# Performance work log

Measured on AMD Instinct MI355X. Metric: run time of the kernel, lower is better.

## Reference

```python
import jax, jax.numpy as jnp
import numpy as np
from jax import lax

B, C, H, W = 4, 64, 256, 256
CH = C // 2  # attention hidden channels


def conv2d_same(x, w, b):
    # x: [B,Ci,H,W], w: [Co,Ci,kh,kw]
    y = lax.conv_general_dilated(x, w, (1, 1), 'SAME',
                                 dimension_numbers=('NCHW', 'OIHW', 'NCHW'))
    return y + b[None, :, None, None]


def conv1x1(x, w):
    # w: [Co,Ci]
    return jnp.einsum('oi,bihw->bohw', w, x)


def irnn_scan(x, w, b, axis, reverse):
    """Directional IRNN: h_t = relu(x_t + w_c * h_{t-1} + b_c), per channel.
    axis: 2 (rows/H) or 3 (cols/W). reverse=True scans from the far edge
    (e.g. bottom-to-top for 'up', right-to-left for 'left')."""
    xs = jnp.moveaxis(x, axis, 0)            # [L, B, C, rest]
    wb = w[None, :, None]                    # broadcast over [B, C, rest]
    bb = b[None, :, None]

    def step(h, xt):
        h = jax.nn.relu(xt + wb * h + bb)
        return h, h

    h0 = jnp.zeros_like(xs[0])
    _, ys = lax.scan(step, h0, xs, reverse=reverse)
    return jnp.moveaxis(ys, 0, axis)


def setup_inputs() -> dict:
    key = jax.random.key(0)
    ks = jax.random.split(key, 16)
    d = {}
    d['x'] = jax.random.normal(ks[0], (B, C, H, W), dtype=jnp.float32)
    # conv_in: 1x1, no bias
    d['w_in'] = jax.random.normal(ks[1], (C, C), dtype=jnp.float32) * 0.05
    # IRNN depthwise 1x1 weights (init alpha=1.0 in torch) + biases
    for i, name in enumerate(['up', 'right', 'down', 'left']):
        d['w_' + name] = jnp.ones((C,), dtype=jnp.float32)
        d['b_' + name] = jax.random.normal(ks[2 + i], (C,), dtype=jnp.float32) * 0.01
    # convD2: 1x1, 4C -> C, no bias
    d['wD2'] = jax.random.normal(ks[6], (C, 4 * C), dtype=jnp.float32) * 0.01
    # attention layers
    d['a1_w'] = jax.random.normal(ks[7], (CH, C, 3, 3), dtype=jnp.float32) * 0.05
    d['a1_b'] = jnp.zeros((CH,), dtype=jnp.float32)
    d['a2_w'] = jax.random.normal(ks[8], (CH, CH, 3, 3), dtype=jnp.float32) * 0.05
    d['a2_b'] = jnp.zeros((CH,), dtype=jnp.float32)
    d['a3_w'] = jax.random.normal(ks[9], (1, CH), dtype=jnp.float32) * 0.05
    d['a3_b'] = jnp.zeros((1,), dtype=jnp.float32)
    return d


def reference(x, w_in, w_up, b_up, w_right, b_right, w_down, b_down,
              w_left, b_left, wD2, a1_w, a1_b, a2_w, a2_b, a3_w, a3_b):
    out = conv1x1(x, w_in)
    # four directional spatial IRNN scans
    top_up = irnn_scan(out, w_up, b_up, axis=2, reverse=True)     # bottom->top
    top_right = irnn_scan(out, w_right, b_right, axis=3, reverse=False)  # left->right
    top_down = irnn_scan(out, w_down, b_down, axis=2, reverse=False)     # top->bottom
    top_left = irnn_scan(out, w_left, b_left, axis=3, reverse=True)      # right->left
    cat = jnp.concatenate([top_up, top_right, top_down, top_left], axis=1)  # [B,4C,H,W]
    out = jax.nn.relu(conv1x1(cat, wD2))
    # attention gate
    a = jax.nn.relu(conv2d_same(out, a1_w, a1_b))
    a = jax.nn.relu(conv2d_same(a, a2_w, a2_b))
    a = conv1x1(a, a3_w) + a3_b[None, :, None, None]
    weight = jax.nn.sigmoid(a)                # [B,1,H,W]
    return jax.nn.relu(x * weight)
```

## Files before the change

### kernel.cpp

```cpp
#include <hip/hip_runtime.h>
#include <hip/hip_bf16.h>

#define HWSZ  65536

typedef unsigned short ushort_t;
typedef unsigned int   uint_t;
typedef __attribute__((ext_vector_type(8))) _Float16 half8;
typedef __attribute__((ext_vector_type(2))) _Float16 half2v;
typedef __attribute__((ext_vector_type(4))) float f32x4;

static __device__ __forceinline__ void gl_lds16(const void* g, void* l) {
    __builtin_amdgcn_global_load_lds(
        (const __attribute__((address_space(1))) unsigned int*)g,
        (__attribute__((address_space(3))) unsigned int*)l, 16, 0, 0);
}

__global__ __launch_bounds__(256) void k1_mfma(
    const float* __restrict__ x, const float* __restrict__ w_in,
    _Float16* __restrict__ out0)
{
    __shared__ float xs[64][64];
    __shared__ _Float16 ah[64][72];
    __shared__ _Float16 al[64][72];
    int b   = blockIdx.x >> 10;
    int hw0 = (blockIdx.x & 1023) << 6;
    const float* xb = x + ((size_t)b * 64) * HWSZ + hw0;
    int wave = threadIdx.x >> 6, lane = threadIdx.x & 63;
    int n16 = lane & 15, quad = lane >> 4;

    for (int idx = threadIdx.x; idx < 1024; idx += 256) {
        int i = idx >> 4, p4 = (idx & 15) << 2;
        *(float4*)&xs[i][p4] = *(const float4*)(xb + (size_t)i * HWSZ + p4);
    }

    half8 Bh[2], Bl[2];
#pragma unroll
    for (int s = 0; s < 2; s++) {
        const float* wp = w_in + (wave * 16 + n16) * 64 + s * 32 + quad * 8;
#pragma unroll
        for (int j = 0; j < 8; j++) {
            float v = wp[j];
            _Float16 h = (_Float16)v;
            float r = v - (float)h;
            Bh[s][j] = h; Bl[s][j] = (_Float16)r;
        }
    }
    __syncthreads();

    {
        int px  = threadIdx.x & 63;
        int ic0 = (threadIdx.x >> 6) << 4;
        half8 h0, h1, l0, l1;
#pragma unroll
        for (int e = 0; e < 8; e++) {
            float v = xs[ic0 + e][px];
            _Float16 h = (_Float16)v;
            h0[e] = h; l0[e] = (_Float16)(v - (float)h);
        }
#pragma unroll
        for (int e = 0; e < 8; e++) {
            float v = xs[ic0 + 8 + e][px];
            _Float16 h = (_Float16)v;
            h1[e] = h; l1[e] = (_Float16)(v - (float)h);
        }
        *(half8*)&ah[px][ic0]     = h0;
        *(half8*)&ah[px][ic0 + 8] = h1;
        *(half8*)&al[px][ic0]     = l0;
        *(half8*)&al[px][ic0 + 8] = l1;
    }
    __syncthreads();

    f32x4 acc[4] = {};
#pragma unroll
    for (int j = 0; j < 4; j++) {
        int px = j * 16 + n16;
#pragma unroll
        for (int s = 0; s < 2; s++) {
            half8 Ah = *(const half8*)&ah[px][s * 32 + quad * 8];
            half8 Al = *(const half8*)&al[px][s * 32 + quad * 8];
            acc[j] = __builtin_amdgcn_mfma_f32_16x16x32_f16(Ah, Bh[s], acc[j], 0, 0, 0);
            acc[j] = __builtin_amdgcn_mfma_f32_16x16x32_f16(Al, Bh[s], acc[j], 0, 0, 0);
            acc[j] = __builtin_amdgcn_mfma_f32_16x16x32_f16(Ah, Bl[s], acc[j], 0, 0, 0);
        }
    }
    _Float16* ob = out0 + ((size_t)b * HWSZ + hw0) * 64 + wave * 16;
#pragma unroll
    for (int j = 0; j < 4; j++)
#pragma unroll
        for (int r = 0; r < 4; r++) {
            int px = j * 16 + quad * 4 + r;
            ob[(size_t)px * 64 + n16] = (_Float16)acc[j][r];
        }
}

__global__ __launch_bounds__(256) void k2_scan(
    const _Float16* __restrict__ out0,
    const float* __restrict__ w_up, const float* __restrict__ b_up,
    const float* __restrict__ w_rt, const float* __restrict__ b_rt,
    const float* __restrict__ w_dn, const float* __restrict__ b_dn,
    const float* __restrict__ w_lf, const float* __restrict__ b_lf,
    _Float16* __restrict__ cat)
{
    int c2 = threadIdx.x & 31;
    int q  = threadIdx.x >> 5;
    int dir = blockIdx.x >> 7;
    int bid = blockIdx.x & 127;
    int b = bid >> 5, g = bid & 31;
    int line = g * 8 + q;
    size_t base = (size_t)b * HWSZ;
    bool vert = dir < 2;
    bool rev  = dir & 1;

    const float *wp, *bp; int coff;
    if      (dir == 0) { wp = w_dn; bp = b_dn; coff = 128; }
    else if (dir == 1) { wp = w_up; bp = b_up; coff = 0;   }
    else if (dir == 2) { wp = w_rt; bp = b_rt; coff = 64;  }
    else               { wp = w_lf; bp = b_lf; coff = 192; }
    float w0v = wp[2 * c2], b0v = bp[2 * c2];
    float w1v = wp[2 * c2 + 1], b1v = bp[2 * c2 + 1];
    int coff2 = coff >> 1;

    const half2v* src = (const half2v*)out0;
    half2v* dst = (half2v*)cat;

    float h0 = 0.f, h1 = 0.f;
    for (int k0 = 0; k0 < 256; k0 += 16) {
        half2v v[16];
#pragma unroll
        for (int jx = 0; jx < 16; jx++) {
            int i = rev ? 255 - (k0 + jx) : (k0 + jx);
            size_t pix = vert ? (base + i * 256 + line) : (base + line * 256 + i);
            v[jx] = src[pix * 32 + c2];
        }
#pragma unroll
        for (int jx = 0; jx < 16; jx++) {
            int i = rev ? 255 - (k0 + jx) : (k0 + jx);
            size_t pix = vert ? (base + i * 256 + line) : (base + line * 256 + i);
            h0 = fmaxf(0.f, (float)v[jx][0] + w0v * h0 + b0v);
            h1 = fmaxf(0.f, (float)v[jx][1] + w1v * h1 + b1v);
            half2v o; o[0] = (_Float16)h0; o[1] = (_Float16)h1;
            dst[pix * 128 + coff2 + c2] = o;
        }
    }
}

__global__ __launch_bounds__(256) void packall(
    const float* __restrict__ wD2, const float* __restrict__ a1w,
    const float* __restrict__ a2w,
    _Float16* __restrict__ wf, _Float16* __restrict__ p1,
    _Float16* __restrict__ p2)
{
    int i = blockIdx.x * 256 + threadIdx.x;
    if (i < 16384) {
        wf[i] = (_Float16)wD2[i];
        return;
    }
    int k = i - 16384;
    if (k < 18432) {
        int j = k & 7, lane = (k >> 3) & 63, st = k >> 9;
        int s = st >> 1, t = st & 1;
        int oc = t * 16 + (lane & 15);
        int gk = s * 32 + (lane >> 4) * 8 + j;
        int dydx = gk >> 6, ic = gk & 63;
        p1[k] = (_Float16)a1w[((oc * 64 + ic) * 3 + dydx / 3) * 3 + dydx % 3];
    } else if (k < 27648) {
        int e = k - 18432;
        int j = e & 7, lane = (e >> 3) & 63, st = e >> 9;
        int s = st >> 1, t = st & 1;
        int oc = t * 16 + (lane & 15);
        int gk = s * 32 + (lane >> 4) * 8 + j;
        int dydx = gk >> 5, ic = gk & 31;
        p2[e] = (_Float16)a2w[((oc * 32 + ic) * 3 + dydx / 3) * 3 + dydx % 3];
    }
}

__global__ __launch_bounds__(256) void k3_mfma(
    const _Float16* __restrict__ cat, const _Float16* __restrict__ wf,
    _Float16* __restrict__ out3)
{
    __shared__ _Float16 As[64 * 256];
    int wave = threadIdx.x >> 6, lane = threadIdx.x & 63;
    int n16 = lane & 15, quad = lane >> 4;
    size_t p0 = (size_t)blockIdx.x * 64;

    half8 B[8];
#pragma unroll
    for (int s = 0; s < 8; s++)
        B[s] = *(const half8*)(wf + (size_t)(wave * 16 + n16) * 256 + s * 32 + quad * 8);

#pragma unroll
    for (int it = 0; it < 8; it++) {
        int px = wave * 16 + it * 2 + (lane >> 5);
        int pu = lane & 31;
        int lu = pu ^ (px & 7);
        const _Float16* gp = cat + ((p0 + px) << 8) + lu * 8;
        _Float16* lp = As + wave * 4096 + it * 512;
        gl_lds16(gp, lp);
    }
    __syncthreads();

    f32x4 acc[4] = {};
#pragma unroll
    for (int j = 0; j < 4; j++) {
        int px = j * 16 + n16;
        const _Float16* lrow = As + px * 256;
        int x7 = px & 7;
#pragma unroll
        for (int s = 0; s < 8; s++) {
            int phys = (s * 4 + quad) ^ x7;
            half8 a = *(const half8*)(lrow + phys * 8);
            acc[j] = __builtin_amdgcn_mfma_f32_16x16x32_f16(a, B[s], acc[j], 0, 0, 0);
        }
    }

#pragma unroll
    for (int j = 0; j < 4; j++)
#pragma unroll
        for (int r = 0; r < 4; r++) {
            size_t op = (p0 + j * 16 + quad * 4 + r) * 64 + wave * 16 + n16;
            out3[op] = (_Float16)fmaxf(acc[j][r], 0.f);
        }
}

template <int IC>
__global__ __launch_bounds__(256) void convmfma(
    const _Float16* __restrict__ in, const _Float16* __restrict__ pb,
    const float* __restrict__ bias, _Float16* __restrict__ oh)
{
    constexpr int UPX = IC / 8;
    constexpr int KST = IC / 32;
    constexpr int PPS = 64 / UPX;
    __shared__ _Float16 Ls[6 * 66 * IC];

    int wave = threadIdx.x >> 6, lane = threadIdx.x & 63;
    int n16 = lane & 15, quad = lane >> 4;
    int bid = blockIdx.x;
    int bb  = bid >> 8;
    int hh0 = ((bid >> 2) & 63) << 2;
    int w0  = (bid & 3) << 6;
    const _Float16* ib = in + (size_t)bb * HWSZ * IC;

#pragma unroll
    for (int it = 0; it < (6 * UPX) / 4; it++) {
        int q   = it * 4 + wave;
        int r   = q / UPX, seg = q % UPX;
        int gh  = hh0 - 1 + r;
        int pxr = seg * PPS + lane / UPX;
        int pu  = lane % UPX;
        int px_lin = r * 66 + 1 + pxr;
        int lu  = (UPX == 8) ? (pu ^ (px_lin & 7)) : pu;
        _Float16* lp = Ls + (size_t)(r * 66 + 1 + seg * PPS) * IC;
        if ((unsigned)gh < 256u) {
            const _Float16* gp = ib + ((size_t)(gh * 256 + w0 + pxr)) * IC + lu * 8;
            gl_lds16(gp, lp);
        } else {
            half8 z = {};
            *(half8*)(lp + (size_t)lane * 8) = z;
        }
    }
    if (threadIdx.x < 12 * UPX) {
        int pu = threadIdx.x % UPX;
        int ph = threadIdx.x / UPX;
        int r = ph >> 1, side = ph & 1;
        int col = side ? 65 : 0;
        int gh = hh0 - 1 + r;
        int gw = w0 - 1 + side * 65;
        int px_lin = r * 66 + col;
        int lu = (UPX == 8) ? (pu ^ (px_lin & 7)) : pu;
        half8 v = {};
        if ((unsigned)gh < 256u && (unsigned)gw < 256u)
            v = *(const half8*)(ib + ((size_t)(gh * 256 + gw)) * IC + lu * 8);
        *(half8*)(Ls + (size_t)px_lin * IC + pu * 8) = v;
    }
    __syncthreads();

    f32x4 acc[4][2] = {};
#pragma unroll
    for (int dydx = 0; dydx < 9; dydx++) {
        int dy = dydx / 3, dx = dydx % 3;
        int r_lds = wave + dy;
#pragma unroll
        for (int kst = 0; kst < KST; kst++) {
            int s = dydx * KST + kst;
            half8 B0 = *(const half8*)(pb + (size_t)((s * 2 + 0) * 64 + lane) * 8);
            half8 B1 = *(const half8*)(pb + (size_t)((s * 2 + 1) * 64 + lane) * 8);
            int u = kst * 4 + quad;
#pragma unroll
            for (int j = 0; j < 4; j++) {
                int px_lin = r_lds * 66 + j * 16 + n16 + dx;
                int phys = (UPX == 8) ? (u ^ (px_lin & 7)) : u;
                half8 A = *(const half8*)(Ls + (size_t)px_lin * IC + phys * 8);
                acc[j][0] = __builtin_amdgcn_mfma_f32_16x16x32_f16(A, B0, acc[j][0], 0, 0, 0);
                acc[j][1] = __builtin_amdgcn_mfma_f32_16x16x32_f16(A, B1, acc[j][1], 0, 0, 0);
            }
        }
    }

    int hh = hh0 + wave;
#pragma unroll
    for (int t = 0; t < 2; t++) {
        float bv = bias[t * 16 + n16];
#pragma unroll
        for (int j = 0; j < 4; j++)
#pragma unroll
            for (int r = 0; r < 4; r++) {
                int wp = w0 + j * 16 + quad * 4 + r;
                size_t op = ((size_t)bb * HWSZ + hh * 256 + wp) * 32 + t * 16 + n16;
                oh[op] = (_Float16)fmaxf(acc[j][t][r] + bv, 0.f);
            }
    }
}

__global__ __launch_bounds__(256) void k6_gate(
    const _Float16* __restrict__ a2, const float* __restrict__ a3w,
    const float* __restrict__ a3b, const float* __restrict__ x,
    float* __restrict__ out)
{
    int pix = blockIdx.x * 256 + threadIdx.x;
    int b = pix >> 16;
    int hw = pix & 65535;
    const _Float16* ap = a2 + (size_t)pix * 32;
    half8 q0 = *(const half8*)(ap);
    half8 q1 = *(const half8*)(ap + 8);
    half8 q2 = *(const half8*)(ap + 16);
    half8 q3 = *(const half8*)(ap + 24);
    float s = a3b[0];
#pragma unroll
    for (int j = 0; j < 8; j++) {
        s += a3w[j]      * (float)q0[j];
        s += a3w[j + 8]  * (float)q1[j];
        s += a3w[j + 16] * (float)q2[j];
        s += a3w[j + 24] * (float)q3[j];
    }
    float g = 1.f / (1.f + __expf(-s));
    const float* xb = x + (size_t)b * 64 * HWSZ + hw;
    float* ob = out + (size_t)b * 64 * HWSZ + hw;
#pragma unroll 8
    for (int c = 0; c < 64; c++)
        ob[(size_t)c * HWSZ] = fmaxf(0.f, xb[(size_t)c * HWSZ] * g);
}

extern "C" void kernel_launch(void* const* d_in, const int* in_sizes, int n_in,
                              void* d_out, int out_size, void* d_ws, size_t ws_size,
                              hipStream_t stream)
{
    const float* x     = (const float*)d_in[0];
    const float* w_in  = (const float*)d_in[1];
    const float* w_up  = (const float*)d_in[2];
    const float* b_up  = (const float*)d_in[3];
    const float* w_rt  = (const float*)d_in[4];
    const float* b_rt  = (const float*)d_in[5];
    const float* w_dn  = (const float*)d_in[6];
    const float* b_dn  = (const float*)d_in[7];
    const float* w_lf  = (const float*)d_in[8];
    const float* b_lf  = (const float*)d_in[9];
    const float* wD2   = (const float*)d_in[10];
    const float* a1w   = (const float*)d_in[11];
    const float* a1b   = (const float*)d_in[12];
    const float* a2w   = (const float*)d_in[13];
    const float* a2b   = (const float*)d_in[14];
    const float* a3w   = (const float*)d_in[15];
    const float* a3b   = (const float*)d_in[16];
    float* out = (float*)d_out;

    char* ws = (char*)d_ws;
    _Float16* out0 = (_Float16*)ws;
    _Float16* out3 = (_Float16*)ws;
    _Float16* wf16 = (_Float16*)(ws + (33ull << 20));
    _Float16* p1   = (_Float16*)(ws + (34ull << 20));
    _Float16* p2   = (_Float16*)(ws + (35ull << 20));
    _Float16* cat  = (_Float16*)(ws + (64ull << 20));
    _Float16* a1   = (_Float16*)(ws + (64ull << 20));
    _Float16* a2   = (_Float16*)(ws + (80ull << 20));

    k1_mfma   <<<4096, 256, 0, stream>>>(x, w_in, out0);
    k2_scan   <<<512,  256, 0, stream>>>(out0, w_up, b_up, w_rt, b_rt,
                                         w_dn, b_dn, w_lf, b_lf, cat);
    packall   <<<172,  256, 0, stream>>>(wD2, a1w, a2w, wf16, p1, p2);
    k3_mfma   <<<4096, 256, 0, stream>>>(cat, wf16, out3);
    convmfma<64><<<1024, 256, 0, stream>>>(out3, p1, a1b, a1);
    convmfma<32><<<1024, 256, 0, stream>>>(a1, p2, a2b, a2);
    k6_gate   <<<1024, 256, 0, stream>>>(a2, a3w, a3b, x, out);
}
```

Before: 268.3 us.

## Parallelize IRNN scan along sequence with chunked max-affine composition

Each scan line is split into 8 chunks of 32 steps, one per wavefront. Each chunk first computes a composable summary of the relu-affine recurrence, h -> max(M, S*h + T), and stores it in LDS. After a barrier, each chunk folds the summaries of the chunks before it to get its starting state, then rescans its 32 steps and writes the outputs. This raises the grid from 512 to 4096 blocks to break the long serial dependency chain, at the cost of reading the input twice. The composition is exact for relu(w*h + x + b), but the float ordering differs slightly from a plain sequential scan.

```diff
diff --git a/kernel.cpp b/kernel.cpp
--- a/kernel.cpp
+++ b/kernel.cpp
@@ -101,12 +101,12 @@
     const float* __restrict__ w_lf, const float* __restrict__ b_lf,
     _Float16* __restrict__ cat)
 {
+    __shared__ float comb[8][32][6];
     int c2 = threadIdx.x & 31;
-    int q  = threadIdx.x >> 5;
-    int dir = blockIdx.x >> 7;
-    int bid = blockIdx.x & 127;
-    int b = bid >> 5, g = bid & 31;
-    int line = g * 8 + q;
+    int ck = threadIdx.x >> 5;
+    int dir  = blockIdx.x >> 10;
+    int b    = (blockIdx.x >> 8) & 3;
+    int line = blockIdx.x & 255;
     size_t base = (size_t)b * HWSZ;
     bool vert = dir < 2;
     bool rev  = dir & 1;
@@ -123,25 +123,44 @@
     const half2v* src = (const half2v*)out0;
     half2v* dst = (half2v*)cat;
 
+#define PIXOF(k) (vert ? (base + (size_t)(rev ? 255 - (k) : (k)) * 256 + line) \
+                       : (base + line * 256 + (size_t)(rev ? 255 - (k) : (k))))
+
+    int k0 = ck << 5;
+
+    float M0 = -3e38f, S0 = 1.f, T0 = 0.f;
+    float M1 = -3e38f, S1 = 1.f, T1 = 0.f;
+#pragma unroll
+    for (int j = 0; j < 32; j++) {
+        half2v v = src[PIXOF(k0 + j) * 32 + c2];
+        float c0 = (float)v[0] + b0v;
+        float c1 = (float)v[1] + b1v;
+        M0 = fmaxf(0.f, fmaf(w0v, M0, c0));
+        T0 = fmaf(w0v, T0, c0);
+        S0 *= w0v;
+        M1 = fmaxf(0.f, fmaf(w1v, M1, c1));
+        T1 = fmaf(w1v, T1, c1);
+        S1 *= w1v;
+    }
+    comb[ck][c2][0] = M0; comb[ck][c2][1] = S0; comb[ck][c2][2] = T0;
+    comb[ck][c2][3] = M1; comb[ck][c2][4] = S1; comb[ck][c2][5] = T1;
+    __syncthreads();
+
     float h0 = 0.f, h1 = 0.f;
-    for (int k0 = 0; k0 < 256; k0 += 16) {
-        half2v v[16];
-#pragma unroll
-        for (int jx = 0; jx < 16; jx++) {
-            int i = rev ? 255 - (k0 + jx) : (k0 + jx);
-            size_t pix = vert ? (base + i * 256 + line) : (base + line * 256 + i);
-            v[jx] = src[pix * 32 + c2];
-        }
-#pragma unroll
-        for (int jx = 0; jx < 16; jx++) {
-            int i = rev ? 255 - (k0 + jx) : (k0 + jx);
-            size_t pix = vert ? (base + i * 256 + line) : (base + line * 256 + i);
-            h0 = fmaxf(0.f, (float)v[jx][0] + w0v * h0 + b0v);
-            h1 = fmaxf(0.f, (float)v[jx][1] + w1v * h1 + b1v);
-            half2v o; o[0] = (_Float16)h0; o[1] = (_Float16)h1;
-            dst[pix * 128 + coff2 + c2] = o;
-        }
-    }
+    for (int j = 0; j < ck; j++) {
+        h0 = fmaxf(comb[j][c2][0], fmaf(comb[j][c2][1], h0, comb[j][c2][2]));
+        h1 = fmaxf(comb[j][c2][3], fmaf(comb[j][c2][4], h1, comb[j][c2][5]));
+    }
+
+#pragma unroll
+    for (int j = 0; j < 32; j++) {
+        half2v v = src[PIXOF(k0 + j) * 32 + c2];
+        h0 = fmaxf(0.f, fmaf(w0v, h0, (float)v[0] + b0v));
+        h1 = fmaxf(0.f, fmaf(w1v, h1, (float)v[1] + b1v));
+        half2v o; o[0] = (_Float16)h0; o[1] = (_Float16)h1;
+        dst[PIXOF(k0 + j) * 128 + coff2 + c2] = o;
+    }
+#undef PIXOF
 }
 
 __global__ __launch_bounds__(256) void packall(
@@ -374,7 +393,7 @@
     _Float16* a2   = (_Float16*)(ws + (80ull << 20));
 
     k1_mfma   <<<4096, 256, 0, stream>>>(x, w_in, out0);
-    k2_scan   <<<512,  256, 0, stream>>>(out0, w_up, b_up, w_rt, b_rt,
+    k2_scan   <<<4096, 256, 0, stream>>>(out0, w_up, b_up, w_rt, b_rt,
                                          w_dn, b_dn, w_lf, b_lf, cat);
     packall   <<<172,  256, 0, stream>>>(wD2, a1w, a2w, wf16, p1, p2);
     k3_mfma   <<<4096, 256, 0, stream>>>(cat, wf16, out3);
```

Measured after the change: 328.6 us. 1.23x slower.
